# Optimization experiments

Measured on AMD Instinct MI355X. Metric: run time of the kernel, lower is better.

The kernel has to match this reference:

```python
import jax, jax.numpy as jnp
import numpy as np

N_NODES = 100000
N_EDGES = 1600000
N_GRAPHS = 64
BN_EPS = 1e-5


def setup_inputs() -> dict:
    key = jax.random.key(0)
    ks = jax.random.split(key, 16)
    inp = {
        'x': jax.random.normal(ks[0], (N_NODES, 768), dtype=jnp.float32),
        'edge_index': jax.random.randint(ks[1], (2, N_EDGES), 0, N_NODES, dtype=jnp.int32),
        'batch': jnp.sort(jax.random.randint(ks[2], (N_NODES,), 0, N_GRAPHS, dtype=jnp.int32)),
        'W_in': jax.random.normal(ks[3], (768, 256), dtype=jnp.float32) * 0.02,
        'b_in': jax.random.normal(ks[4], (256,), dtype=jnp.float32) * 0.02,
        'W_g': jax.random.normal(ks[5], (3, 256, 256), dtype=jnp.float32) * 0.05,
        'b_g': jax.random.normal(ks[6], (3, 256), dtype=jnp.float32) * 0.02,
        'bn_gamma': jax.random.uniform(ks[7], (3, 256), dtype=jnp.float32) + 0.5,
        'bn_beta': jax.random.normal(ks[8], (3, 256), dtype=jnp.float32) * 0.02,
        'bn_mean': jax.random.normal(ks[9], (3, 256), dtype=jnp.float32) * 0.02,
        'bn_var': jax.random.uniform(ks[10], (3, 256), dtype=jnp.float32) + 0.5,
        'W1': jax.random.normal(ks[11], (256, 128), dtype=jnp.float32) * 0.06,
        'b1': jax.random.normal(ks[12], (128,), dtype=jnp.float32) * 0.02,
        'W2': jax.random.normal(ks[13], (128, 128), dtype=jnp.float32) * 0.08,
        'b2': jax.random.normal(ks[14], (128,), dtype=jnp.float32) * 0.02,
    }
    return inp


def reference(x, edge_index, batch, W_in, b_in, W_g, b_g, bn_gamma, bn_beta,
              bn_mean, bn_var, W1, b1, W2, b2):
    N = x.shape[0]
    # Add self loops (PyG GCNConv default)
    loop = jnp.arange(N, dtype=edge_index.dtype)
    src = jnp.concatenate([edge_index[0], loop])  # [E+N]
    dst = jnp.concatenate([edge_index[1], loop])
    # Symmetric GCN normalization: deg over dst after self loops
    deg = jax.ops.segment_sum(jnp.ones_like(src, dtype=x.dtype), dst, num_segments=N)
    dinv = jnp.where(deg > 0, jax.lax.rsqrt(deg), 0.0)
    norm = (dinv[src] * dinv[dst])[:, None]  # [E+N, 1]

    # input projection + relu
    h = jax.nn.relu(x @ W_in + b_in)  # [N, 256]

    for i in range(W_g.shape[0]):
        m = h @ W_g[i]                                   # [N, 256]
        agg = jax.ops.segment_sum(m[src] * norm, dst, num_segments=N) + b_g[i]
        # BatchNorm (eval mode, running stats)
        agg = (agg - bn_mean[i]) * (bn_gamma[i] * jax.lax.rsqrt(bn_var[i] + BN_EPS)) + bn_beta[i]
        h = jax.nn.relu(agg)  # dropout is identity in eval

    # global mean pool per graph
    sums = jax.ops.segment_sum(h, batch, num_segments=N_GRAPHS)       # [G, 256]
    cnts = jax.ops.segment_sum(jnp.ones((N,), x.dtype), batch, num_segments=N_GRAPHS)
    g = sums / jnp.maximum(cnts, 1.0)[:, None]

    # output MLP
    out = jax.nn.relu(g @ W1 + b1) @ W2 + b2  # [G, 128]
    return out
```

## Files before the change

### kernel.cpp

```cpp
#include <hip/hip_runtime.h>
#include <hip/hip_fp16.h>

#define HIDDEN 256

using bfrag = __attribute__((ext_vector_type(8))) short;
using facc4 = __attribute__((ext_vector_type(4))) float;

__device__ inline short bf16_rne(float x) {
  unsigned u = __builtin_bit_cast(unsigned, x);
  unsigned r = u + 0x7FFFu + ((u >> 16) & 1u);
  return (short)(r >> 16);
}
__device__ inline float bf16_to_f(short h) {
  unsigned u = ((unsigned)(unsigned short)h) << 16;
  return __builtin_bit_cast(float, u);
}
__device__ inline float h2f(unsigned short h) {
  return __half2float(__builtin_bit_cast(__half, h));
}
__device__ inline void cvt8(const float4& a, const float4& b, bfrag& hi, bfrag& lo) {
  float av[8] = {a.x, a.y, a.z, a.w, b.x, b.y, b.z, b.w};
#pragma unroll
  for (int i = 0; i < 8; ++i) {
    unsigned u = __builtin_bit_cast(unsigned, av[i]);
    hi[i] = (short)(u >> 16);
    float r = av[i] - __builtin_bit_cast(float, u & 0xFFFF0000u);
    lo[i] = (short)(__builtin_bit_cast(unsigned, r) >> 16);
  }
}

__global__ __launch_bounds__(256) void k_hist(const int* __restrict__ dst,
                                              int* __restrict__ deg, int E) {
  for (int e = blockIdx.x * blockDim.x + threadIdx.x; e < E;
       e += gridDim.x * blockDim.x)
    atomicAdd(&deg[dst[e]], 1);
}

__global__ __launch_bounds__(256) void k_scan_a(const int* __restrict__ deg,
                                                int* __restrict__ bsum, int N) {
  const int t = threadIdx.x, lane = t & 63, w = t >> 6;
  const int idx = blockIdx.x * 256 + t;
  int x = (idx < N) ? deg[idx] : 0;
#pragma unroll
  for (int off = 32; off >= 1; off >>= 1) x += __shfl_xor(x, off);
  __shared__ int ws[4];
  if (lane == 0) ws[w] = x;
  __syncthreads();
  if (t == 0) bsum[blockIdx.x] = ws[0] + ws[1] + ws[2] + ws[3];
}

__global__ __launch_bounds__(512) void k_scan_b(const int* __restrict__ bsum,
                                                int* __restrict__ boff, int nb) {
  const int t = threadIdx.x, lane = t & 63, w = t >> 6;
  int orig = (t < nb) ? bsum[t] : 0;
  int x = orig;
#pragma unroll
  for (int off = 1; off < 64; off <<= 1) {
    int y = __shfl_up(x, off);
    if (lane >= off) x += y;
  }
  __shared__ int wsum[8];
  if (lane == 63) wsum[w] = x;
  __syncthreads();
  if (w == 0 && lane < 8) {
    int s = wsum[lane];
#pragma unroll
    for (int off = 1; off < 8; off <<= 1) {
      int y = __shfl_up(s, off);
      if (lane >= off) s += y;
    }
    wsum[lane] = s;
  }
  __syncthreads();
  int inc = x + (w > 0 ? wsum[w - 1] : 0);
  if (t < nb) boff[t] = inc - orig;
}

__global__ __launch_bounds__(256) void k_scan_c(const int* __restrict__ deg,
                                                const int* __restrict__ boff,
                                                int* __restrict__ row_ptr,
                                                float* __restrict__ dinv, int N) {
  const int t = threadIdx.x, lane = t & 63, w = t >> 6;
  const int idx = blockIdx.x * 256 + t;
  int d = (idx < N) ? deg[idx] : 0;
  int x = d;
#pragma unroll
  for (int off = 1; off < 64; off <<= 1) {
    int y = __shfl_up(x, off);
    if (lane >= off) x += y;
  }
  __shared__ int ws[4];
  if (lane == 63) ws[w] = x;
  __syncthreads();
  int add = boff[blockIdx.x];
#pragma unroll
  for (int j = 0; j < 4; ++j)
    if (j < w) add += ws[j];
  if (idx < N) {
    row_ptr[idx + 1] = x + add;
    dinv[idx] = 1.0f / sqrtf((float)d + 1.0f);
  }
  if (idx == 0) row_ptr[0] = 0;
}

__global__ __launch_bounds__(256) void k_fill(const int* __restrict__ src,
                                              const int* __restrict__ dst,
                                              const int* __restrict__ row_ptr,
                                              int* __restrict__ fill,
                                              int* __restrict__ csr, int E) {
  for (int e = blockIdx.x * blockDim.x + threadIdx.x; e < E;
       e += gridDim.x * blockDim.x) {
    int d = dst[e];
    int pos = atomicAdd(&fill[d], 1);
    csr[row_ptr[d] + pos] = src[e];
  }
}

__global__ __launch_bounds__(256) void k_prep_w(const float* __restrict__ W_in,
                                                const float* __restrict__ W_g,
                                                short* __restrict__ Wt) {
  const int e = blockIdx.x * blockDim.x + threadIdx.x;
  if (e >= 196608 + 3 * 65536) return;
  float v;
  int k, n;
  size_t base;
  if (e < 196608) {
    k = e >> 8;
    n = e & 255;
    v = W_in[e];
    base = 0;
  } else {
    int r = e - 196608;
    int lyr = r >> 16;
    k = (r >> 8) & 255;
    n = r & 255;
    v = W_g[r];
    base = 393216 + (size_t)lyr * 131072;
  }
  size_t pos = base + (size_t)(k >> 5) * 16384 + (size_t)n * 32 + (k & 31);
  short hi = bf16_rne(v);
  short lo = bf16_rne(v - bf16_to_f(hi));
  Wt[pos] = hi;
  Wt[pos + 8192] = lo;
}

template <int EPI>
__global__ __launch_bounds__(512, 4) void gemm_mfma(const float* __restrict__ A,
                                                    const short* __restrict__ Wt,
                                                    const float* __restrict__ aux,
                                                    float* __restrict__ C,
                                                    int M, int K) {
  __shared__ short As[2][128][72];
  const int t = threadIdx.x;
  const int w = t >> 6, l = t & 63;
  const int g = l >> 4, m16 = l & 15;
  const int wr = w >> 2, wc = w & 3;
  const int row0 = blockIdx.x * 128;
  const int arow = t >> 2;
  const int ks = (t & 3) << 3;

  facc4 acc[4][4];
#pragma unroll
  for (int i = 0; i < 4; ++i)
#pragma unroll
    for (int j = 0; j < 4; ++j) acc[i][j] = (facc4)(0.0f);

  const int nsteps = K >> 5;
  const int ga = row0 + arow;
  const bool aval = ga < M;
  const float* aptr = A + (size_t)ga * K + ks;

  float4 f0 = make_float4(0.f, 0.f, 0.f, 0.f), f1 = f0;
  if (aval) {
    f0 = *(const float4*)(aptr + 0);
    f1 = *(const float4*)(aptr + 4);
  }
  {
    bfrag hi, lo;
    cvt8(f0, f1, hi, lo);
    *(bfrag*)&As[0][arow][ks] = hi;
    *(bfrag*)&As[0][arow][32 + ks] = lo;
  }

  int cur = 0;
  for (int s = 0; s < nsteps; ++s) {
    __syncthreads();
    const bool havenext = (s + 1 < nsteps);
    if (havenext && aval) {
      const float* ap = aptr + (size_t)(s + 1) * 32;
      f0 = *(const float4*)(ap + 0);
      f1 = *(const float4*)(ap + 4);
    }
    const short* wb = Wt + ((size_t)s << 14) + (size_t)(wc * 64 + m16) * 32 + g * 8;
    bfrag bh[4], bl[4];
#pragma unroll
    for (int nf = 0; nf < 4; ++nf) {
      bh[nf] = *(const bfrag*)(wb + nf * 512);
      bl[nf] = *(const bfrag*)(wb + nf * 512 + 8192);
    }
    bfrag af[4];
#pragma unroll
    for (int mf = 0; mf < 4; ++mf)
      af[mf] = *(const bfrag*)&As[cur][wr * 64 + mf * 16 + m16][g * 8];
#pragma unroll
    for (int nf = 0; nf < 4; ++nf)
#pragma unroll
      for (int mf = 0; mf < 4; ++mf)
        acc[mf][nf] = __builtin_amdgcn_mfma_f32_16x16x32_bf16(
            af[mf], bh[nf], acc[mf][nf], 0, 0, 0);
#pragma unroll
    for (int nf = 0; nf < 4; ++nf)
#pragma unroll
      for (int mf = 0; mf < 4; ++mf)
        acc[mf][nf] = __builtin_amdgcn_mfma_f32_16x16x32_bf16(
            af[mf], bl[nf], acc[mf][nf], 0, 0, 0);
#pragma unroll
    for (int mf = 0; mf < 4; ++mf)
      af[mf] = *(const bfrag*)&As[cur][wr * 64 + mf * 16 + m16][32 + g * 8];
#pragma unroll
    for (int nf = 0; nf < 4; ++nf)
#pragma unroll
      for (int mf = 0; mf < 4; ++mf)
        acc[mf][nf] = __builtin_amdgcn_mfma_f32_16x16x32_bf16(
            af[mf], bh[nf], acc[mf][nf], 0, 0, 0);
    if (havenext) {
      bfrag hi, lo;
      cvt8(f0, f1, hi, lo);
      *(bfrag*)&As[cur ^ 1][arow][ks] = hi;
      *(bfrag*)&As[cur ^ 1][arow][32 + ks] = lo;
    }
    cur ^= 1;
  }
  const int colbase = wc * 64;
  const int rowbase = row0 + wr * 64;
  if (EPI == 0) {
#pragma unroll
    for (int nf = 0; nf < 4; ++nf) {
      const float bias = aux[colbase + nf * 16 + m16];
#pragma unroll
      for (int mf = 0; mf < 4; ++mf)
#pragma unroll
        for (int r = 0; r < 4; ++r) {
          int row = rowbase + mf * 16 + g * 4 + r;
          if (row < M)
            C[(size_t)row * HIDDEN + colbase + nf * 16 + m16] =
                fmaxf(acc[mf][nf][r] + bias, 0.f);
        }
    }
  } else {
    __half* Ch = (__half*)C;
#pragma unroll
    for (int mf = 0; mf < 4; ++mf)
#pragma unroll
      for (int r = 0; r < 4; ++r) {
        int row = rowbase + mf * 16 + g * 4 + r;
        if (row >= M) continue;
        const float sc = aux[row];
#pragma unroll
        for (int nf = 0; nf < 4; ++nf)
          Ch[(size_t)row * HIDDEN + colbase + nf * 16 + m16] =
              __float2half(acc[mf][nf][r] * sc);
      }
  }
}

__global__ __launch_bounds__(256) void k_aggregate(
    const unsigned short* __restrict__ mp, const int* __restrict__ row_ptr,
    const int* __restrict__ csr, const float* __restrict__ dinv,
    const float* __restrict__ bg, const float* __restrict__ gamma,
    const float* __restrict__ beta, const float* __restrict__ mean,
    const float* __restrict__ var, float* __restrict__ hout, int N) {
  const int wave = threadIdx.x >> 6, l = threadIdx.x & 63;
  const int v = blockIdx.x * 4 + wave;
  if (v >= N) return;
  const int co = l << 2;
  ushort4 rs = *(const ushort4*)(mp + (size_t)v * HIDDEN + co);
  float4 acc;
  acc.x = h2f(rs.x); acc.y = h2f(rs.y); acc.z = h2f(rs.z); acc.w = h2f(rs.w);
  const int s = row_ptr[v], e = row_ptr[v + 1];
  int i = s;
  for (; i + 8 <= e; i += 8) {
    ushort4 r0 = *(const ushort4*)(mp + (size_t)csr[i + 0] * HIDDEN + co);
    ushort4 r1 = *(const ushort4*)(mp + (size_t)csr[i + 1] * HIDDEN + co);
    ushort4 r2 = *(const ushort4*)(mp + (size_t)csr[i + 2] * HIDDEN + co);
    ushort4 r3 = *(const ushort4*)(mp + (size_t)csr[i + 3] * HIDDEN + co);
    ushort4 r4 = *(const ushort4*)(mp + (size_t)csr[i + 4] * HIDDEN + co);
    ushort4 r5 = *(const ushort4*)(mp + (size_t)csr[i + 5] * HIDDEN + co);
    ushort4 r6 = *(const ushort4*)(mp + (size_t)csr[i + 6] * HIDDEN + co);
    ushort4 r7 = *(const ushort4*)(mp + (size_t)csr[i + 7] * HIDDEN + co);
    acc.x += h2f(r0.x) + h2f(r1.x) + h2f(r2.x) + h2f(r3.x) +
             h2f(r4.x) + h2f(r5.x) + h2f(r6.x) + h2f(r7.x);
    acc.y += h2f(r0.y) + h2f(r1.y) + h2f(r2.y) + h2f(r3.y) +
             h2f(r4.y) + h2f(r5.y) + h2f(r6.y) + h2f(r7.y);
    acc.z += h2f(r0.z) + h2f(r1.z) + h2f(r2.z) + h2f(r3.z) +
             h2f(r4.z) + h2f(r5.z) + h2f(r6.z) + h2f(r7.z);
    acc.w += h2f(r0.w) + h2f(r1.w) + h2f(r2.w) + h2f(r3.w) +
             h2f(r4.w) + h2f(r5.w) + h2f(r6.w) + h2f(r7.w);
  }
  for (; i < e; ++i) {
    ushort4 r0 = *(const ushort4*)(mp + (size_t)csr[i] * HIDDEN + co);
    acc.x += h2f(r0.x);
    acc.y += h2f(r0.y);
    acc.z += h2f(r0.z);
    acc.w += h2f(r0.w);
  }
  const float dv = dinv[v];
  float4 bg4 = *(const float4*)&bg[co];
  float4 g4 = *(const float4*)&gamma[co];
  float4 be4 = *(const float4*)&beta[co];
  float4 mn4 = *(const float4*)&mean[co];
  float4 vr4 = *(const float4*)&var[co];
  float4 o;
  o.x = fmaxf((acc.x * dv + bg4.x - mn4.x) * (g4.x / sqrtf(vr4.x + 1e-5f)) + be4.x, 0.f);
  o.y = fmaxf((acc.y * dv + bg4.y - mn4.y) * (g4.y / sqrtf(vr4.y + 1e-5f)) + be4.y, 0.f);
  o.z = fmaxf((acc.z * dv + bg4.z - mn4.z) * (g4.z / sqrtf(vr4.z + 1e-5f)) + be4.z, 0.f);
  o.w = fmaxf((acc.w * dv + bg4.w - mn4.w) * (g4.w / sqrtf(vr4.w + 1e-5f)) + be4.w, 0.f);
  ((float4*)hout)[(size_t)v * 64 + l] = o;
}

__global__ __launch_bounds__(64) void k_count(const int* __restrict__ batch,
                                              float* __restrict__ cnt, int N,
                                              int G) {
  const int g = threadIdx.x;
  if (g >= G) return;
  int lo = 0, hi = N;
  while (lo < hi) {
    int mid = (lo + hi) >> 1;
    if (batch[mid] < g) lo = mid + 1; else hi = mid;
  }
  int lo2 = lo, hi2 = N;
  while (lo2 < hi2) {
    int mid = (lo2 + hi2) >> 1;
    if (batch[mid] < g + 1) lo2 = mid + 1; else hi2 = mid;
  }
  cnt[g] = (float)(lo2 - lo);
}

__global__ __launch_bounds__(256) void k_pool(const float* __restrict__ h,
                                              const int* __restrict__ batch,
                                              float* __restrict__ sums, int N) {
  const int t = threadIdx.x;
  const int start = blockIdx.x * 256;
  if (start >= N) return;
  const int end = min(start + 256, N);
  float acc = 0.f;
  int cur = batch[start];
  for (int n = start; n < end; ++n) {
    int g = batch[n];
    if (g != cur) {
      atomicAdd(&sums[cur * HIDDEN + t], acc);
      acc = 0.f;
      cur = g;
    }
    acc += h[(size_t)n * HIDDEN + t];
  }
  atomicAdd(&sums[cur * HIDDEN + t], acc);
}

__global__ __launch_bounds__(128) void k_head(const float* __restrict__ sums,
                                              const float* __restrict__ cnt,
                                              const float* __restrict__ W1,
                                              const float* __restrict__ b1,
                                              const float* __restrict__ W2,
                                              const float* __restrict__ b2,
                                              float* __restrict__ out) {
  __shared__ float gr[256];
  __shared__ float t1[128];
  const int b = blockIdx.x, t = threadIdx.x;
  const float inv = 1.0f / fmaxf(cnt[b], 1.0f);
  gr[t] = sums[b * HIDDEN + t] * inv;
  gr[t + 128] = sums[b * HIDDEN + t + 128] * inv;
  __syncthreads();
  float a = b1[t];
  for (int k = 0; k < 256; ++k) a += gr[k] * W1[k * 128 + t];
  t1[t] = fmaxf(a, 0.f);
  __syncthreads();
  float o = b2[t];
  for (int k = 0; k < 128; ++k) o += t1[k] * W2[k * 128 + t];
  out[b * 128 + t] = o;
}

extern "C" void kernel_launch(void* const* d_in, const int* in_sizes, int n_in,
                              void* d_out, int out_size, void* d_ws,
                              size_t ws_size, hipStream_t stream) {
  (void)n_in;
  (void)ws_size;
  const float* x = (const float*)d_in[0];
  const int* ei = (const int*)d_in[1];
  const int* batch = (const int*)d_in[2];
  const float* W_in = (const float*)d_in[3];
  const float* b_in = (const float*)d_in[4];
  const float* W_g = (const float*)d_in[5];
  const float* b_g = (const float*)d_in[6];
  const float* bn_gamma = (const float*)d_in[7];
  const float* bn_beta = (const float*)d_in[8];
  const float* bn_mean = (const float*)d_in[9];
  const float* bn_var = (const float*)d_in[10];
  const float* W1 = (const float*)d_in[11];
  const float* b1 = (const float*)d_in[12];
  const float* W2 = (const float*)d_in[13];
  const float* b2 = (const float*)d_in[14];

  const int KIN = 768;
  const int N = in_sizes[0] / KIN;
  const int E = in_sizes[1] / 2;
  const int G = out_size / 128;

  const int* src = ei;
  const int* dst = ei + E;

  char* ws = (char*)d_ws;
  size_t off = 0;
  auto take = [&](size_t bytes) -> void* {
    void* p = ws + off;
    off += (bytes + 255) & ~(size_t)255;
    return p;
  };
  float* h0 = (float*)take((size_t)N * HIDDEN * 4);
  unsigned short* h1 = (unsigned short*)take((size_t)N * HIDDEN * 2);
  float* dinv = (float*)take((size_t)N * 4);
  int* deg = (int*)take((size_t)N * 4);
  int* fill = (int*)take((size_t)N * 4);
  int* row_ptr = (int*)take((size_t)(N + 1) * 4);
  int* csr = (int*)take((size_t)E * 4);
  float* sums = (float*)take((size_t)G * HIDDEN * 4);
  float* cnt = (float*)take((size_t)G * 4);
  short* Wt = (short*)take((size_t)(393216 + 3 * 131072) * 2);
  const int nb = (N + 255) / 256;
  int* bsum = (int*)take((size_t)nb * 4);
  int* boff = (int*)take((size_t)nb * 4);

  hipMemsetAsync(deg, 0, (size_t)N * 4, stream);
  hipMemsetAsync(fill, 0, (size_t)N * 4, stream);
  hipMemsetAsync(sums, 0, (size_t)G * HIDDEN * 4, stream);

  k_prep_w<<<(196608 + 3 * 65536 + 255) / 256, 256, 0, stream>>>(W_in, W_g, Wt);
  k_hist<<<2048, 256, 0, stream>>>(dst, deg, E);
  k_scan_a<<<nb, 256, 0, stream>>>(deg, bsum, N);
  k_scan_b<<<1, 512, 0, stream>>>(bsum, boff, nb);
  k_scan_c<<<nb, 256, 0, stream>>>(deg, boff, row_ptr, dinv, N);
  k_fill<<<2048, 256, 0, stream>>>(src, dst, row_ptr, fill, csr, E);

  const int gx = (N + 127) / 128;
  gemm_mfma<0><<<gx, 512, 0, stream>>>(x, Wt, b_in, h0, N, KIN);
  for (int i = 0; i < 3; ++i) {
    gemm_mfma<1><<<gx, 512, 0, stream>>>(h0, Wt + 393216 + (size_t)i * 131072,
                                         dinv, (float*)h1, N, HIDDEN);
    k_aggregate<<<(N + 3) / 4, 256, 0, stream>>>(
        h1, row_ptr, csr, dinv, b_g + i * HIDDEN, bn_gamma + i * HIDDEN,
        bn_beta + i * HIDDEN, bn_mean + i * HIDDEN, bn_var + i * HIDDEN, h0, N);
  }
  k_count<<<1, 64, 0, stream>>>(batch, cnt, N, G);
  k_pool<<<(N + 255) / 256, 256, 0, stream>>>(h0, batch, sums, N);
  k_head<<<G, 128, 0, stream>>>(sums, cnt, W1, b1, W2, b2, (float*)d_out);
}
```

Measured before the change: 1.161 ms.

## Store activations as packed bf16 hi/lo pairs and drop LDS staging in GEMM

Hidden activations are now written by the input GEMM and the aggregate kernel as packed bf16 hi/lo pairs, so the layer GEMMs load ready-made MFMA fragments instead of converting fp32. The GEMM loses its shared-memory double buffer: each 256-thread block covers 64 rows, and every wave reads its A fragments straight from global memory while owning 64 output columns. This removes LDS traffic, barriers and per-step conversion in the layer GEMMs. In exchange, each A row is fetched redundantly by all four waves, global loads are strided per lane, and the pooling kernel has to unpack the pairs.

```diff
diff --git a/kernel.cpp b/kernel.cpp
--- a/kernel.cpp
+++ b/kernel.cpp
@@ -27,6 +27,13 @@
     float r = av[i] - __builtin_bit_cast(float, u & 0xFFFF0000u);
     lo[i] = (short)(__builtin_bit_cast(unsigned, r) >> 16);
   }
+}
+__device__ inline unsigned packsplit(float v) {
+  unsigned u = __builtin_bit_cast(unsigned, v);
+  unsigned hi = u >> 16;
+  float r = v - __builtin_bit_cast(float, u & 0xFFFF0000u);
+  unsigned lo = __builtin_bit_cast(unsigned, r) >> 16;
+  return hi | (lo << 16);
 }
 
 __global__ __launch_bounds__(256) void k_hist(const int* __restrict__ dst,
@@ -144,20 +151,17 @@
   Wt[pos + 8192] = lo;
 }
 
-template <int EPI>
-__global__ __launch_bounds__(512, 4) void gemm_mfma(const float* __restrict__ A,
+template <int MODE>
+__global__ __launch_bounds__(256, 3) void gemm_mfma(const void* __restrict__ Ain,
                                                     const short* __restrict__ Wt,
                                                     const float* __restrict__ aux,
-                                                    float* __restrict__ C,
+                                                    void* __restrict__ Cout,
                                                     int M, int K) {
-  __shared__ short As[2][128][72];
   const int t = threadIdx.x;
   const int w = t >> 6, l = t & 63;
   const int g = l >> 4, m16 = l & 15;
-  const int wr = w >> 2, wc = w & 3;
-  const int row0 = blockIdx.x * 128;
-  const int arow = t >> 2;
-  const int ks = (t & 3) << 3;
+  const int row0 = blockIdx.x * 64;
+  const int colbase = w * 64;
 
   facc4 acc[4][4];
 #pragma unroll
@@ -165,75 +169,81 @@
 #pragma unroll
     for (int j = 0; j < 4; ++j) acc[i][j] = (facc4)(0.0f);
 
+  int rowm[4];
+#pragma unroll
+  for (int mf = 0; mf < 4; ++mf) {
+    int r = row0 + mf * 16 + m16;
+    rowm[mf] = (r < M) ? r : (M - 1);
+  }
+
   const int nsteps = K >> 5;
-  const int ga = row0 + arow;
-  const bool aval = ga < M;
-  const float* aptr = A + (size_t)ga * K + ks;
-
-  float4 f0 = make_float4(0.f, 0.f, 0.f, 0.f), f1 = f0;
-  if (aval) {
-    f0 = *(const float4*)(aptr + 0);
-    f1 = *(const float4*)(aptr + 4);
-  }
-  {
-    bfrag hi, lo;
-    cvt8(f0, f1, hi, lo);
-    *(bfrag*)&As[0][arow][ks] = hi;
-    *(bfrag*)&As[0][arow][32 + ks] = lo;
-  }
-
-  int cur = 0;
+  const short* wb = Wt + (size_t)(colbase + m16) * 32 + g * 8;
+
   for (int s = 0; s < nsteps; ++s) {
-    __syncthreads();
-    const bool havenext = (s + 1 < nsteps);
-    if (havenext && aval) {
-      const float* ap = aptr + (size_t)(s + 1) * 32;
-      f0 = *(const float4*)(ap + 0);
-      f1 = *(const float4*)(ap + 4);
+    bfrag ah[4], al[4], bh[4], bl[4];
+    if (MODE == 0) {
+      const float* A = (const float*)Ain;
+      float4 f0[4], f1[4];
+#pragma unroll
+      for (int mf = 0; mf < 4; ++mf) {
+        const float* p = A + (size_t)rowm[mf] * K + s * 32 + g * 8;
+        f0[mf] = *(const float4*)p;
+        f1[mf] = *(const float4*)(p + 4);
+      }
+#pragma unroll
+      for (int nf = 0; nf < 4; ++nf) {
+        bh[nf] = *(const bfrag*)(wb + nf * 512);
+        bl[nf] = *(const bfrag*)(wb + nf * 512 + 8192);
+      }
+#pragma unroll
+      for (int mf = 0; mf < 4; ++mf) cvt8(f0[mf], f1[mf], ah[mf], al[mf]);
+    } else {
+      const unsigned* A = (const unsigned*)Ain;
+      uint4 u0[4], u1[4];
+#pragma unroll
+      for (int mf = 0; mf < 4; ++mf) {
+        const unsigned* p = A + (size_t)rowm[mf] * K + s * 32 + g * 8;
+        u0[mf] = *(const uint4*)p;
+        u1[mf] = *(const uint4*)(p + 4);
+      }
+#pragma unroll
+      for (int nf = 0; nf < 4; ++nf) {
+        bh[nf] = *(const bfrag*)(wb + nf * 512);
+        bl[nf] = *(const bfrag*)(wb + nf * 512 + 8192);
+      }
+#pragma unroll
+      for (int mf = 0; mf < 4; ++mf) {
+        unsigned uu[8] = {u0[mf].x, u0[mf].y, u0[mf].z, u0[mf].w,
+                          u1[mf].x, u1[mf].y, u1[mf].z, u1[mf].w};
+#pragma unroll
+        for (int j = 0; j < 8; ++j) {
+          ah[mf][j] = (short)(uu[j] & 0xFFFFu);
+          al[mf][j] = (short)(uu[j] >> 16);
+        }
+      }
     }
-    const short* wb = Wt + ((size_t)s << 14) + (size_t)(wc * 64 + m16) * 32 + g * 8;
-    bfrag bh[4], bl[4];
-#pragma unroll
-    for (int nf = 0; nf < 4; ++nf) {
-      bh[nf] = *(const bfrag*)(wb + nf * 512);
-      bl[nf] = *(const bfrag*)(wb + nf * 512 + 8192);
-    }
-    bfrag af[4];
-#pragma unroll
-    for (int mf = 0; mf < 4; ++mf)
-      af[mf] = *(const bfrag*)&As[cur][wr * 64 + mf * 16 + m16][g * 8];
+    wb += 16384;
 #pragma unroll
     for (int nf = 0; nf < 4; ++nf)
 #pragma unroll
       for (int mf = 0; mf < 4; ++mf)
         acc[mf][nf] = __builtin_amdgcn_mfma_f32_16x16x32_bf16(
-            af[mf], bh[nf], acc[mf][nf], 0, 0, 0);
+            ah[mf], bh[nf], acc[mf][nf], 0, 0, 0);
 #pragma unroll
     for (int nf = 0; nf < 4; ++nf)
 #pragma unroll
       for (int mf = 0; mf < 4; ++mf)
         acc[mf][nf] = __builtin_amdgcn_mfma_f32_16x16x32_bf16(
-            af[mf], bl[nf], acc[mf][nf], 0, 0, 0);
-#pragma unroll
-    for (int mf = 0; mf < 4; ++mf)
-      af[mf] = *(const bfrag*)&As[cur][wr * 64 + mf * 16 + m16][32 + g * 8];
+            ah[mf], bl[nf], acc[mf][nf], 0, 0, 0);
 #pragma unroll
     for (int nf = 0; nf < 4; ++nf)
 #pragma unroll
       for (int mf = 0; mf < 4; ++mf)
         acc[mf][nf] = __builtin_amdgcn_mfma_f32_16x16x32_bf16(
-            af[mf], bh[nf], acc[mf][nf], 0, 0, 0);
-    if (havenext) {
-      bfrag hi, lo;
-      cvt8(f0, f1, hi, lo);
-      *(bfrag*)&As[cur ^ 1][arow][ks] = hi;
-      *(bfrag*)&As[cur ^ 1][arow][32 + ks] = lo;
-    }
-    cur ^= 1;
-  }
-  const int colbase = wc * 64;
-  const int rowbase = row0 + wr * 64;
-  if (EPI == 0) {
+            al[mf], bh[nf], acc[mf][nf], 0, 0, 0);
+  }
+  if (MODE == 0) {
+    unsigned* Cp = (unsigned*)Cout;
 #pragma unroll
     for (int nf = 0; nf < 4; ++nf) {
       const float bias = aux[colbase + nf * 16 + m16];
@@ -241,19 +251,19 @@
       for (int mf = 0; mf < 4; ++mf)
 #pragma unroll
         for (int r = 0; r < 4; ++r) {
-          int row = rowbase + mf * 16 + g * 4 + r;
+          int row = row0 + mf * 16 + g * 4 + r;
           if (row < M)
-            C[(size_t)row * HIDDEN + colbase + nf * 16 + m16] =
-                fmaxf(acc[mf][nf][r] + bias, 0.f);
+            Cp[(size_t)row * HIDDEN + colbase + nf * 16 + m16] =
+                packsplit(fmaxf(acc[mf][nf][r] + bias, 0.f));
         }
     }
   } else {
-    __half* Ch = (__half*)C;
+    __half* Ch = (__half*)Cout;
 #pragma unroll
     for (int mf = 0; mf < 4; ++mf)
 #pragma unroll
       for (int r = 0; r < 4; ++r) {
-        int row = rowbase + mf * 16 + g * 4 + r;
+        int row = row0 + mf * 16 + g * 4 + r;
         if (row >= M) continue;
         const float sc = aux[row];
 #pragma unroll
@@ -269,7 +279,7 @@
     const int* __restrict__ csr, const float* __restrict__ dinv,
     const float* __restrict__ bg, const float* __restrict__ gamma,
     const float* __restrict__ beta, const float* __restrict__ mean,
-    const float* __restrict__ var, float* __restrict__ hout, int N) {
+    const float* __restrict__ var, unsigned* __restrict__ hout, int N) {
   const int wave = threadIdx.x >> 6, l = threadIdx.x & 63;
   const int v = blockIdx.x * 4 + wave;
   if (v >= N) return;
@@ -310,12 +320,12 @@
   float4 be4 = *(const float4*)&beta[co];
   float4 mn4 = *(const float4*)&mean[co];
   float4 vr4 = *(const float4*)&var[co];
-  float4 o;
-  o.x = fmaxf((acc.x * dv + bg4.x - mn4.x) * (g4.x / sqrtf(vr4.x + 1e-5f)) + be4.x, 0.f);
-  o.y = fmaxf((acc.y * dv + bg4.y - mn4.y) * (g4.y / sqrtf(vr4.y + 1e-5f)) + be4.y, 0.f);
-  o.z = fmaxf((acc.z * dv + bg4.z - mn4.z) * (g4.z / sqrtf(vr4.z + 1e-5f)) + be4.z, 0.f);
-  o.w = fmaxf((acc.w * dv + bg4.w - mn4.w) * (g4.w / sqrtf(vr4.w + 1e-5f)) + be4.w, 0.f);
-  ((float4*)hout)[(size_t)v * 64 + l] = o;
+  uint4 o;
+  o.x = packsplit(fmaxf((acc.x * dv + bg4.x - mn4.x) * (g4.x / sqrtf(vr4.x + 1e-5f)) + be4.x, 0.f));
+  o.y = packsplit(fmaxf((acc.y * dv + bg4.y - mn4.y) * (g4.y / sqrtf(vr4.y + 1e-5f)) + be4.y, 0.f));
+  o.z = packsplit(fmaxf((acc.z * dv + bg4.z - mn4.z) * (g4.z / sqrtf(vr4.z + 1e-5f)) + be4.z, 0.f));
+  o.w = packsplit(fmaxf((acc.w * dv + bg4.w - mn4.w) * (g4.w / sqrtf(vr4.w + 1e-5f)) + be4.w, 0.f));
+  *(uint4*)&hout[(size_t)v * HIDDEN + co] = o;
 }
 
 __global__ __launch_bounds__(64) void k_count(const int* __restrict__ batch,
@@ -336,7 +346,7 @@
   cnt[g] = (float)(lo2 - lo);
 }
 
-__global__ __launch_bounds__(256) void k_pool(const float* __restrict__ h,
+__global__ __launch_bounds__(256) void k_pool(const unsigned* __restrict__ h,
                                               const int* __restrict__ batch,
                                               float* __restrict__ sums, int N) {
   const int t = threadIdx.x;
@@ -352,7 +362,8 @@
       acc = 0.f;
       cur = g;
     }
-    acc += h[(size_t)n * HIDDEN + t];
+    unsigned u = h[(size_t)n * HIDDEN + t];
+    acc += bf16_to_f((short)(u & 0xFFFFu)) + bf16_to_f((short)(u >> 16));
   }
   atomicAdd(&sums[cur * HIDDEN + t], acc);
 }
@@ -416,7 +427,7 @@
     off += (bytes + 255) & ~(size_t)255;
     return p;
   };
-  float* h0 = (float*)take((size_t)N * HIDDEN * 4);
+  unsigned* h0 = (unsigned*)take((size_t)N * HIDDEN * 4);
   unsigned short* h1 = (unsigned short*)take((size_t)N * HIDDEN * 2);
   float* dinv = (float*)take((size_t)N * 4);
   int* deg = (int*)take((size_t)N * 4);
@@ -441,11 +452,11 @@
   k_scan_c<<<nb, 256, 0, stream>>>(deg, boff, row_ptr, dinv, N);
   k_fill<<<2048, 256, 0, stream>>>(src, dst, row_ptr, fill, csr, E);
 
-  const int gx = (N + 127) / 128;
-  gemm_mfma<0><<<gx, 512, 0, stream>>>(x, Wt, b_in, h0, N, KIN);
+  const int gx = (N + 63) / 64;
+  gemm_mfma<0><<<gx, 256, 0, stream>>>(x, Wt, b_in, h0, N, KIN);
   for (int i = 0; i < 3; ++i) {
-    gemm_mfma<1><<<gx, 512, 0, stream>>>(h0, Wt + 393216 + (size_t)i * 131072,
-                                         dinv, (float*)h1, N, HIDDEN);
+    gemm_mfma<1><<<gx, 256, 0, stream>>>(h0, Wt + 393216 + (size_t)i * 131072,
+                                         dinv, h1, N, HIDDEN);
     k_aggregate<<<(N + 3) / 4, 256, 0, stream>>>(
         h1, row_ptr, csr, dinv, b_g + i * HIDDEN, bn_gamma + i * HIDDEN,
         bn_beta + i * HIDDEN, bn_mean + i * HIDDEN, bn_var + i * HIDDEN, h0, N);
```

After: 1.220 ms. 1.05x slower.

## Restructure GEMM to 64-row tiles with register double-buffered weight fragments

Applied to the files above, without the earlier changes.

Shrinks the GEMM block from 128 to 64 rows and from 512 to 256 threads, so each wave owns a 64-column slice of the output. The K loop is unrolled by two, and weight fragments are prefetched into two register sets one step ahead of the MFMAs that use them. Barriers now wait only on LDS and scalar-memory counters. The aim is to hide global weight-load latency and cut how many waves stall at barriers. In exchange, each block reads every weight tile for only 64 rows, which doubles total weight traffic, and the extra fragment registers raise register pressure.

```diff
diff --git a/kernel.cpp b/kernel.cpp
--- a/kernel.cpp
+++ b/kernel.cpp
@@ -5,6 +5,12 @@
 
 using bfrag = __attribute__((ext_vector_type(8))) short;
 using facc4 = __attribute__((ext_vector_type(4))) float;
+
+#define BARRIER_LGKM()                                   \
+  do {                                                   \
+    asm volatile("s_waitcnt lgkmcnt(0)" ::: "memory");   \
+    __builtin_amdgcn_s_barrier();                        \
+  } while (0)
 
 __device__ inline short bf16_rne(float x) {
   unsigned u = __builtin_bit_cast(unsigned, x);
@@ -144,20 +150,32 @@
   Wt[pos + 8192] = lo;
 }
 
+#define MFMA_PASSES(AH, AL, BH, BL)                                        \
+  _Pragma("unroll") for (int nf = 0; nf < 4; ++nf)                         \
+      _Pragma("unroll") for (int mf = 0; mf < 4; ++mf) acc[mf][nf] =       \
+      __builtin_amdgcn_mfma_f32_16x16x32_bf16(AH[mf], BH[nf], acc[mf][nf], \
+                                              0, 0, 0);                    \
+  _Pragma("unroll") for (int nf = 0; nf < 4; ++nf)                         \
+      _Pragma("unroll") for (int mf = 0; mf < 4; ++mf) acc[mf][nf] =       \
+      __builtin_amdgcn_mfma_f32_16x16x32_bf16(AH[mf], BL[nf], acc[mf][nf], \
+                                              0, 0, 0);                    \
+  _Pragma("unroll") for (int nf = 0; nf < 4; ++nf)                         \
+      _Pragma("unroll") for (int mf = 0; mf < 4; ++mf) acc[mf][nf] =       \
+      __builtin_amdgcn_mfma_f32_16x16x32_bf16(AL[mf], BH[nf], acc[mf][nf], \
+                                              0, 0, 0);
+
 template <int EPI>
-__global__ __launch_bounds__(512, 4) void gemm_mfma(const float* __restrict__ A,
+__global__ __launch_bounds__(256, 2) void gemm_mfma(const float* __restrict__ A,
                                                     const short* __restrict__ Wt,
                                                     const float* __restrict__ aux,
                                                     float* __restrict__ C,
                                                     int M, int K) {
-  __shared__ short As[2][128][72];
+  __shared__ short As[2][64][66];
   const int t = threadIdx.x;
   const int w = t >> 6, l = t & 63;
   const int g = l >> 4, m16 = l & 15;
-  const int wr = w >> 2, wc = w & 3;
-  const int row0 = blockIdx.x * 128;
-  const int arow = t >> 2;
-  const int ks = (t & 3) << 3;
+  const int row0 = blockIdx.x * 64;
+  const int arow = t >> 2, ak = (t & 3) << 3;
 
   facc4 acc[4][4];
 #pragma unroll
@@ -168,71 +186,92 @@
   const int nsteps = K >> 5;
   const int ga = row0 + arow;
   const bool aval = ga < M;
-  const float* aptr = A + (size_t)ga * K + ks;
+  const float* aptr = A + (size_t)ga * K + ak;
+  const short* wbbase = Wt + (size_t)(w * 64 + m16) * 32 + g * 8;
 
   float4 f0 = make_float4(0.f, 0.f, 0.f, 0.f), f1 = f0;
   if (aval) {
-    f0 = *(const float4*)(aptr + 0);
+    f0 = *(const float4*)aptr;
     f1 = *(const float4*)(aptr + 4);
   }
   {
     bfrag hi, lo;
     cvt8(f0, f1, hi, lo);
-    *(bfrag*)&As[0][arow][ks] = hi;
-    *(bfrag*)&As[0][arow][32 + ks] = lo;
-  }
-
-  int cur = 0;
-  for (int s = 0; s < nsteps; ++s) {
-    __syncthreads();
-    const bool havenext = (s + 1 < nsteps);
-    if (havenext && aval) {
-      const float* ap = aptr + (size_t)(s + 1) * 32;
-      f0 = *(const float4*)(ap + 0);
-      f1 = *(const float4*)(ap + 4);
-    }
-    const short* wb = Wt + ((size_t)s << 14) + (size_t)(wc * 64 + m16) * 32 + g * 8;
-    bfrag bh[4], bl[4];
-#pragma unroll
-    for (int nf = 0; nf < 4; ++nf) {
-      bh[nf] = *(const bfrag*)(wb + nf * 512);
-      bl[nf] = *(const bfrag*)(wb + nf * 512 + 8192);
-    }
-    bfrag af[4];
-#pragma unroll
-    for (int mf = 0; mf < 4; ++mf)
-      af[mf] = *(const bfrag*)&As[cur][wr * 64 + mf * 16 + m16][g * 8];
-#pragma unroll
-    for (int nf = 0; nf < 4; ++nf)
-#pragma unroll
-      for (int mf = 0; mf < 4; ++mf)
-        acc[mf][nf] = __builtin_amdgcn_mfma_f32_16x16x32_bf16(
-            af[mf], bh[nf], acc[mf][nf], 0, 0, 0);
-#pragma unroll
-    for (int nf = 0; nf < 4; ++nf)
-#pragma unroll
-      for (int mf = 0; mf < 4; ++mf)
-        acc[mf][nf] = __builtin_amdgcn_mfma_f32_16x16x32_bf16(
-            af[mf], bl[nf], acc[mf][nf], 0, 0, 0);
-#pragma unroll
-    for (int mf = 0; mf < 4; ++mf)
-      af[mf] = *(const bfrag*)&As[cur][wr * 64 + mf * 16 + m16][32 + g * 8];
-#pragma unroll
-    for (int nf = 0; nf < 4; ++nf)
-#pragma unroll
-      for (int mf = 0; mf < 4; ++mf)
-        acc[mf][nf] = __builtin_amdgcn_mfma_f32_16x16x32_bf16(
-            af[mf], bh[nf], acc[mf][nf], 0, 0, 0);
-    if (havenext) {
+    *(bfrag*)&As[0][arow][ak] = hi;
+    *(bfrag*)&As[0][arow][32 + ak] = lo;
+  }
+  bfrag bh0[4], bl0[4], bh1[4], bl1[4];
+#pragma unroll
+  for (int nf = 0; nf < 4; ++nf) {
+    bh0[nf] = *(const bfrag*)(wbbase + nf * 512);
+    bl0[nf] = *(const bfrag*)(wbbase + nf * 512 + 8192);
+  }
+  if (nsteps > 1 && aval) {
+    f0 = *(const float4*)(aptr + 32);
+    f1 = *(const float4*)(aptr + 36);
+  }
+
+  for (int s = 0; s < nsteps; s += 2) {
+    BARRIER_LGKM();
+    {
+      const short* wb = wbbase + ((size_t)(s + 1) << 14);
+#pragma unroll
+      for (int nf = 0; nf < 4; ++nf) {
+        bh1[nf] = *(const bfrag*)(wb + nf * 512);
+        bl1[nf] = *(const bfrag*)(wb + nf * 512 + 8192);
+      }
+    }
+    {
+      bfrag ah[4], al[4];
+#pragma unroll
+      for (int mf = 0; mf < 4; ++mf) {
+        ah[mf] = *(const bfrag*)&As[0][mf * 16 + m16][g * 8];
+        al[mf] = *(const bfrag*)&As[0][mf * 16 + m16][32 + g * 8];
+      }
+      MFMA_PASSES(ah, al, bh0, bl0);
+    }
+    {
       bfrag hi, lo;
       cvt8(f0, f1, hi, lo);
-      *(bfrag*)&As[cur ^ 1][arow][ks] = hi;
-      *(bfrag*)&As[cur ^ 1][arow][32 + ks] = lo;
-    }
-    cur ^= 1;
-  }
-  const int colbase = wc * 64;
-  const int rowbase = row0 + wr * 64;
+      *(bfrag*)&As[1][arow][ak] = hi;
+      *(bfrag*)&As[1][arow][32 + ak] = lo;
+    }
+    if (s + 2 < nsteps && aval) {
+      const float* ap = aptr + (size_t)(s + 2) * 32;
+      f0 = *(const float4*)ap;
+      f1 = *(const float4*)(ap + 4);
+    }
+    BARRIER_LGKM();
+    if (s + 2 < nsteps) {
+      const short* wb = wbbase + ((size_t)(s + 2) << 14);
+#pragma unroll
+      for (int nf = 0; nf < 4; ++nf) {
+        bh0[nf] = *(const bfrag*)(wb + nf * 512);
+        bl0[nf] = *(const bfrag*)(wb + nf * 512 + 8192);
+      }
+    }
+    {
+      bfrag ah[4], al[4];
+#pragma unroll
+      for (int mf = 0; mf < 4; ++mf) {
+        ah[mf] = *(const bfrag*)&As[1][mf * 16 + m16][g * 8];
+        al[mf] = *(const bfrag*)&As[1][mf * 16 + m16][32 + g * 8];
+      }
+      MFMA_PASSES(ah, al, bh1, bl1);
+    }
+    if (s + 2 < nsteps) {
+      bfrag hi, lo;
+      cvt8(f0, f1, hi, lo);
+      *(bfrag*)&As[0][arow][ak] = hi;
+      *(bfrag*)&As[0][arow][32 + ak] = lo;
+      if (s + 3 < nsteps && aval) {
+        const float* ap = aptr + (size_t)(s + 3) * 32;
+        f0 = *(const float4*)ap;
+        f1 = *(const float4*)(ap + 4);
+      }
+    }
+  }
+  const int colbase = w * 64;
   if (EPI == 0) {
 #pragma unroll
     for (int nf = 0; nf < 4; ++nf) {
@@ -241,7 +280,7 @@
       for (int mf = 0; mf < 4; ++mf)
 #pragma unroll
         for (int r = 0; r < 4; ++r) {
-          int row = rowbase + mf * 16 + g * 4 + r;
+          int row = row0 + mf * 16 + g * 4 + r;
           if (row < M)
             C[(size_t)row * HIDDEN + colbase + nf * 16 + m16] =
                 fmaxf(acc[mf][nf][r] + bias, 0.f);
@@ -253,7 +292,7 @@
     for (int mf = 0; mf < 4; ++mf)
 #pragma unroll
       for (int r = 0; r < 4; ++r) {
-        int row = rowbase + mf * 16 + g * 4 + r;
+        int row = row0 + mf * 16 + g * 4 + r;
         if (row >= M) continue;
         const float sc = aux[row];
 #pragma unroll
@@ -441,10 +480,10 @@
   k_scan_c<<<nb, 256, 0, stream>>>(deg, boff, row_ptr, dinv, N);
   k_fill<<<2048, 256, 0, stream>>>(src, dst, row_ptr, fill, csr, E);
 
-  const int gx = (N + 127) / 128;
-  gemm_mfma<0><<<gx, 512, 0, stream>>>(x, Wt, b_in, h0, N, KIN);
+  const int gx = (N + 63) / 64;
+  gemm_mfma<0><<<gx, 256, 0, stream>>>(x, Wt, b_in, h0, N, KIN);
   for (int i = 0; i < 3; ++i) {
-    gemm_mfma<1><<<gx, 512, 0, stream>>>(h0, Wt + 393216 + (size_t)i * 131072,
+    gemm_mfma<1><<<gx, 256, 0, stream>>>(h0, Wt + 393216 + (size_t)i * 131072,
                                          dinv, (float*)h1, N, HIDDEN);
     k_aggregate<<<(N + 3) / 4, 256, 0, stream>>>(
         h1, row_ptr, csr, dinv, b_g + i * HIDDEN, bn_gamma + i * HIDDEN,
```

Result: faster. 1.038 ms (-10.6%).
